# Performance work log

Hardware: AMD Instinct MI355X
Metric: run time of the kernel (lower is better)

Reference implementation:

```python
import jax, jax.numpy as jnp
import numpy as np

D = 2048
N_HID = 512
ATT = 512
BATCH = 256
L = 196


def setup_inputs() -> dict:
    key = jax.random.key(0)
    ks = jax.random.split(key, 8)
    s = 0.02
    return {
        "feature": jax.random.normal(ks[0], (BATCH, L, D), dtype=jnp.float32),
        "prev_h": jax.random.normal(ks[1], (BATCH, N_HID), dtype=jnp.float32),
        "W_enc": jax.random.normal(ks[2], (D, ATT), dtype=jnp.float32) * s,
        "b_enc": jnp.zeros((ATT,), dtype=jnp.float32),
        "W_dec": jax.random.normal(ks[3], (N_HID, ATT), dtype=jnp.float32) * s,
        "b_dec": jnp.zeros((ATT,), dtype=jnp.float32),
        "W_tot": jax.random.normal(ks[4], (ATT, 1), dtype=jnp.float32) * s,
        "b_tot": jnp.zeros((1,), dtype=jnp.float32),
    }


def reference(feature, prev_h, W_enc, b_enc, W_dec, b_dec, W_tot, b_tot):
    # att1: (N, L, A); att2: (N, A)
    att1 = jnp.einsum("nld,da->nla", feature, W_enc) + b_enc
    att2 = prev_h @ W_dec + b_dec
    att = jax.nn.relu(att1 + att2[:, None, :])          # (N, L, A)
    scores = (att @ W_tot)[..., 0] + b_tot[0]           # (N, L)
    alpha = jax.nn.softmax(scores, axis=1)              # (N, L)
    weighted_feature = jnp.einsum("nld,nl->nd", feature, alpha)  # (N, D)
    return weighted_feature, alpha
```

## Files before the change

### kernel.cpp

```cpp
#include <hip/hip_runtime.h>
#include <hip/hip_bf16.h>


typedef unsigned short u16;
typedef __attribute__((ext_vector_type(8))) short short8;
typedef __attribute__((ext_vector_type(4))) float f32x4;

#define BATCH 256
#define LQ    196
#define DDIM  2048
#define ADIM  512
#define MTOT  (BATCH * LQ)
#define WF_N  (BATCH * DDIM)
#define KQP   1032

__device__ __forceinline__ ushort4 cvt4(float4 f) {
  ushort4 r;
  r.x = __builtin_bit_cast(u16, (__bf16)f.x);
  r.y = __builtin_bit_cast(u16, (__bf16)f.y);
  r.z = __builtin_bit_cast(u16, (__bf16)f.z);
  r.w = __builtin_bit_cast(u16, (__bf16)f.w);
  return r;
}

__device__ __forceinline__ void glds16(const u16* g, u16* l) {
  __builtin_amdgcn_global_load_lds(
      (const __attribute__((address_space(1))) unsigned int*)g,
      (__attribute__((address_space(3))) unsigned int*)l, 16, 0, 0);
}

__global__ void prep_k(const float* __restrict__ W_enc, u16* __restrict__ Bst,
                       const float* __restrict__ prev_h,
                       const float* __restrict__ W_dec,
                       const float* __restrict__ b_dec,
                       const float* __restrict__ b_enc,
                       float* __restrict__ att2,
                       float* __restrict__ scores) {
  const int b = blockIdx.x, tid = threadIdx.x;
  __shared__ u16 smem[32 * 520];
  if (b < 64) {
    const int ks = b;
    for (int i4 = tid; i4 < 4096; i4 += 256) {
      int dl = i4 >> 7;
      int nn = (i4 & 127) << 2;
      float4 f = *(const float4*)(W_enc + (size_t)(ks * 32 + dl) * 512 + nn);
      *(ushort4*)(&smem[dl * 520 + nn]) = cvt4(f);
    }
    __syncthreads();
    for (int idx = tid; idx < 16384; idx += 256) {
      int kq = idx >> 12;
      int n  = (idx >> 3) & 511;
      int e  = idx & 7;
      Bst[(size_t)ks * 16384 + idx] = smem[(kq * 8 + e) * 520 + n];
    }
  } else if (b < 576) {
    const int n  = (b - 64) >> 1;
    const int c0 = ((b - 64) & 1) << 8;
    float* ph = (float*)smem;
    ph[tid]       = prev_h[n * 512 + tid];
    ph[tid + 256] = prev_h[n * 512 + tid + 256];
    __syncthreads();
    float a0 = b_dec[c0 + tid] + b_enc[c0 + tid];
    #pragma unroll 8
    for (int h = 0; h < 512; h++)
      a0 = fmaf(ph[h], W_dec[h * 512 + c0 + tid], a0);
    att2[n * 512 + c0 + tid] = a0;
  } else {
    scores[(b - 576) * 256 + tid] = 0.f;
  }
}

__global__ __launch_bounds__(256, 4) void score_gemm_k(
    const float* __restrict__ feature, const u16* __restrict__ Bst,
    const float* __restrict__ att2, const float* __restrict__ W_tot,
    float* __restrict__ scores) {
  __shared__ __align__(16) u16 sA[2][4 * KQP];
  __shared__ __align__(16) u16 sB[2][4 * KQP];
  __shared__ float sRed[2][128];

  const int tid = threadIdx.x;
  const int b = blockIdx.x;
  const int mt = (b >> 5) * 8 + (b & 7);
  const int nt = (b >> 3) & 3;
  const int r0 = mt << 7, n0 = nt << 7;
  const int wid = tid >> 6, lane = tid & 63;
  const int wgm = wid >> 1, wgn = wid & 1;
  const int quad = lane >> 4, cid = lane & 15;

  const int arow = tid >> 3, akk4 = tid & 7;
  const float* gA = feature + (size_t)(r0 + arow) * 2048 + akk4 * 4;
  const int wAoff = (akk4 >> 1) * KQP + (arow << 3) + ((akk4 & 1) << 2);

  const u16* gBlane = Bst + (size_t)wid * 4096 + ((size_t)n0 << 3) + lane * 8;

  const int abase = quad * KQP + (((wgm << 6) + cid) << 3);
  const int bbase = quad * KQP + (((wgn << 6) + cid) << 3);

  f32x4 zero = {0.f, 0.f, 0.f, 0.f};
  f32x4 acc[4][4];
  #pragma unroll
  for (int i = 0; i < 4; i++)
    #pragma unroll
    for (int j = 0; j < 4; j++) acc[i][j] = zero;

  float4 a0, a1, a2, a3;
  {
    const float* p = gA;
    a0 = *(const float4*)(p);
    a1 = *(const float4*)(p + 32 * 2048);
    a2 = *(const float4*)(p + 64 * 2048);
    a3 = *(const float4*)(p + 96 * 2048);
    u16* dst = &sB[0][wid * KQP];
    glds16(gBlane, dst);
    glds16(gBlane + 512, dst + 512);
  }

  for (int ks = 0; ks < 64; ks++) {
    const int buf = ks & 1;
    u16* wa = &sA[buf][wAoff];
    *(ushort4*)(wa)       = cvt4(a0);
    *(ushort4*)(wa + 256) = cvt4(a1);
    *(ushort4*)(wa + 512) = cvt4(a2);
    *(ushort4*)(wa + 768) = cvt4(a3);
    __syncthreads();

    if (ks < 63) {
      const float* p = gA + (ks + 1) * 32;
      a0 = *(const float4*)(p);
      a1 = *(const float4*)(p + 32 * 2048);
      a2 = *(const float4*)(p + 64 * 2048);
      a3 = *(const float4*)(p + 96 * 2048);
      const u16* src = gBlane + (size_t)(ks + 1) * 16384;
      u16* dst = &sB[buf ^ 1][wid * KQP];
      glds16(src, dst);
      glds16(src + 512, dst + 512);
    }

    const u16* sa = &sA[buf][abase];
    const u16* sb = &sB[buf][bbase];
    short8 af[4], bfr[4];
    #pragma unroll
    for (int mi = 0; mi < 4; mi++)
      af[mi] = *(const short8*)(sa + (mi << 7));
    #pragma unroll
    for (int ni = 0; ni < 4; ni++)
      bfr[ni] = *(const short8*)(sb + (ni << 7));
    #pragma unroll
    for (int mi = 0; mi < 4; mi++)
      #pragma unroll
      for (int ni = 0; ni < 4; ni++)
        acc[mi][ni] = __builtin_amdgcn_mfma_f32_16x16x32_bf16(
            af[mi], bfr[ni], acc[mi][ni], 0, 0, 0);
  }

  float wt[4];
  #pragma unroll
  for (int ni = 0; ni < 4; ni++)
    wt[ni] = W_tot[n0 + (wgn << 6) + ni * 16 + cid];

  #pragma unroll
  for (int mi = 0; mi < 4; mi++) {
    #pragma unroll
    for (int reg = 0; reg < 4; reg++) {
      int row_local = (wgm << 6) + mi * 16 + quad * 4 + reg;
      int row_flat = r0 + row_local;
      int nb = row_flat / 196;
      const float* a2r = att2 + nb * 512 + n0 + (wgn << 6);
      float s = 0.f;
      #pragma unroll
      for (int ni = 0; ni < 4; ni++) {
        float v = acc[mi][ni][reg] + a2r[ni * 16 + cid];
        s += fmaxf(v, 0.f) * wt[ni];
      }
      s += __shfl_xor(s, 1); s += __shfl_xor(s, 2);
      s += __shfl_xor(s, 4); s += __shfl_xor(s, 8);
      if (cid == 0) sRed[wgn][row_local] = s;
    }
  }
  __syncthreads();
  if (tid < 128) atomicAdd(&scores[r0 + tid], sRed[0][tid] + sRed[1][tid]);
}

__global__ void softmax_k(const float* __restrict__ scores,
                          float* __restrict__ alpha) {
  const int n = blockIdx.x, tid = threadIdx.x;
  __shared__ float red[8];
  float s = (tid < LQ) ? scores[n * LQ + tid] : -1e30f;
  float m = s;
  for (int o = 32; o; o >>= 1) m = fmaxf(m, __shfl_xor(m, o));
  if ((tid & 63) == 0) red[tid >> 6] = m;
  __syncthreads();
  m = fmaxf(fmaxf(red[0], red[1]), fmaxf(red[2], red[3]));
  float e = (tid < LQ) ? __expf(s - m) : 0.f;
  float t = e;
  for (int o = 32; o; o >>= 1) t += __shfl_xor(t, o);
  if ((tid & 63) == 0) red[4 + (tid >> 6)] = t;
  __syncthreads();
  t = red[4] + red[5] + red[6] + red[7];
  if (tid < LQ) alpha[n * LQ + tid] = e / t;
}

__global__ void wsum_k(const float* __restrict__ feature,
                       const float* __restrict__ alpha,
                       float* __restrict__ out) {
  const int n = blockIdx.x >> 1, half = blockIdx.x & 1;
  const int tid = threadIdx.x;
  __shared__ float al[LQ];
  if (tid < LQ) al[tid] = alpha[n * LQ + tid];
  __syncthreads();
  const float* fp = feature + (size_t)n * LQ * DDIM + half * 1024 + tid * 4;
  float4 acc = {0.f, 0.f, 0.f, 0.f};
  #pragma unroll 8
  for (int l = 0; l < LQ; l++) {
    float a = al[l];
    float4 f = *(const float4*)(fp + (size_t)l * DDIM);
    acc.x = fmaf(a, f.x, acc.x); acc.y = fmaf(a, f.y, acc.y);
    acc.z = fmaf(a, f.z, acc.z); acc.w = fmaf(a, f.w, acc.w);
  }
  *(float4*)(out + n * DDIM + half * 1024 + tid * 4) = acc;
}

extern "C" void kernel_launch(void* const* d_in, const int* in_sizes, int n_in,
                              void* d_out, int out_size, void* d_ws, size_t ws_size,
                              hipStream_t stream) {
  const float* feature = (const float*)d_in[0];
  const float* prev_h  = (const float*)d_in[1];
  const float* W_enc   = (const float*)d_in[2];
  const float* b_enc   = (const float*)d_in[3];
  const float* W_dec   = (const float*)d_in[4];
  const float* b_dec   = (const float*)d_in[5];
  const float* W_tot   = (const float*)d_in[6];

  float* out   = (float*)d_out;
  float* wf    = out;
  float* alpha = out + WF_N;

  char* ws = (char*)d_ws;
  u16*   Bst    = (u16*)ws;
  float* att2   = (float*)(ws + (2u << 20));
  float* scores = (float*)(ws + (2u << 20) + (512u << 10));

  prep_k<<<772, 256, 0, stream>>>(W_enc, Bst, prev_h, W_dec, b_dec, b_enc,
                                  att2, scores);
  score_gemm_k<<<1568, 256, 0, stream>>>(feature, Bst, att2, W_tot, scores);
  softmax_k<<<256, 256, 0, stream>>>(scores, alpha);
  wsum_k<<<512, 256, 0, stream>>>(feature, alpha, wf);
}
```

Baseline: 751.5 us.

## Load A operand directly into MFMA registers, bypassing shared memory staging

The feature (A) tile no longer goes through LDS. Each lane now loads its own MFMA fragment rows straight from global memory into registers and converts them to bf16 in place, which removes the LDS writes and reads for A. The cost is duplicated global reads: each feature row is fetched by both wgn warps, so L2/global traffic for A doubles. Register pressure also rises, which is why launch bounds drop occupancy from 4 to 3 blocks per SM.

Result: slower. 1.142 ms (+52.0%).

```diff
diff --git a/kernel.cpp b/kernel.cpp
--- a/kernel.cpp
+++ b/kernel.cpp
@@ -20,6 +20,19 @@
   r.y = __builtin_bit_cast(u16, (__bf16)f.y);
   r.z = __builtin_bit_cast(u16, (__bf16)f.z);
   r.w = __builtin_bit_cast(u16, (__bf16)f.w);
+  return r;
+}
+
+__device__ __forceinline__ short8 cvt8(float4 a, float4 b) {
+  short8 r;
+  r[0] = (short)__builtin_bit_cast(u16, (__bf16)a.x);
+  r[1] = (short)__builtin_bit_cast(u16, (__bf16)a.y);
+  r[2] = (short)__builtin_bit_cast(u16, (__bf16)a.z);
+  r[3] = (short)__builtin_bit_cast(u16, (__bf16)a.w);
+  r[4] = (short)__builtin_bit_cast(u16, (__bf16)b.x);
+  r[5] = (short)__builtin_bit_cast(u16, (__bf16)b.y);
+  r[6] = (short)__builtin_bit_cast(u16, (__bf16)b.z);
+  r[7] = (short)__builtin_bit_cast(u16, (__bf16)b.w);
   return r;
 }
 
@@ -70,11 +83,10 @@
   }
 }
 
-__global__ __launch_bounds__(256, 4) void score_gemm_k(
+__global__ __launch_bounds__(256, 3) void score_gemm_k(
     const float* __restrict__ feature, const u16* __restrict__ Bst,
     const float* __restrict__ att2, const float* __restrict__ W_tot,
     float* __restrict__ scores) {
-  __shared__ __align__(16) u16 sA[2][4 * KQP];
   __shared__ __align__(16) u16 sB[2][4 * KQP];
   __shared__ float sRed[2][128];
 
@@ -87,13 +99,11 @@
   const int wgm = wid >> 1, wgn = wid & 1;
   const int quad = lane >> 4, cid = lane & 15;
 
-  const int arow = tid >> 3, akk4 = tid & 7;
-  const float* gA = feature + (size_t)(r0 + arow) * 2048 + akk4 * 4;
-  const int wAoff = (akk4 >> 1) * KQP + (arow << 3) + ((akk4 & 1) << 2);
+  const float* gAf =
+      feature + (size_t)(r0 + (wgm << 6) + cid) * 2048 + (quad << 3);
 
   const u16* gBlane = Bst + (size_t)wid * 4096 + ((size_t)n0 << 3) + lane * 8;
 
-  const int abase = quad * KQP + (((wgm << 6) + cid) << 3);
   const int bbase = quad * KQP + (((wgn << 6) + cid) << 3);
 
   f32x4 zero = {0.f, 0.f, 0.f, 0.f};
@@ -103,13 +113,16 @@
     #pragma unroll
     for (int j = 0; j < 4; j++) acc[i][j] = zero;
 
-  float4 a0, a1, a2, a3;
+  float4 aF0, aF1, aF2, aF3, aF4, aF5, aF6, aF7;
   {
-    const float* p = gA;
-    a0 = *(const float4*)(p);
-    a1 = *(const float4*)(p + 32 * 2048);
-    a2 = *(const float4*)(p + 64 * 2048);
-    a3 = *(const float4*)(p + 96 * 2048);
+    aF0 = *(const float4*)(gAf);
+    aF1 = *(const float4*)(gAf + 4);
+    aF2 = *(const float4*)(gAf + 16 * 2048);
+    aF3 = *(const float4*)(gAf + 16 * 2048 + 4);
+    aF4 = *(const float4*)(gAf + 32 * 2048);
+    aF5 = *(const float4*)(gAf + 32 * 2048 + 4);
+    aF6 = *(const float4*)(gAf + 48 * 2048);
+    aF7 = *(const float4*)(gAf + 48 * 2048 + 4);
     u16* dst = &sB[0][wid * KQP];
     glds16(gBlane, dst);
     glds16(gBlane + 512, dst + 512);
@@ -117,31 +130,32 @@
 
   for (int ks = 0; ks < 64; ks++) {
     const int buf = ks & 1;
-    u16* wa = &sA[buf][wAoff];
-    *(ushort4*)(wa)       = cvt4(a0);
-    *(ushort4*)(wa + 256) = cvt4(a1);
-    *(ushort4*)(wa + 512) = cvt4(a2);
-    *(ushort4*)(wa + 768) = cvt4(a3);
     __syncthreads();
 
+    short8 af[4];
+    af[0] = cvt8(aF0, aF1);
+    af[1] = cvt8(aF2, aF3);
+    af[2] = cvt8(aF4, aF5);
+    af[3] = cvt8(aF6, aF7);
+
     if (ks < 63) {
-      const float* p = gA + (ks + 1) * 32;
-      a0 = *(const float4*)(p);
-      a1 = *(const float4*)(p + 32 * 2048);
-      a2 = *(const float4*)(p + 64 * 2048);
-      a3 = *(const float4*)(p + 96 * 2048);
+      const float* p = gAf + (ks + 1) * 32;
+      aF0 = *(const float4*)(p);
+      aF1 = *(const float4*)(p + 4);
+      aF2 = *(const float4*)(p + 16 * 2048);
+      aF3 = *(const float4*)(p + 16 * 2048 + 4);
+      aF4 = *(const float4*)(p + 32 * 2048);
+      aF5 = *(const float4*)(p + 32 * 2048 + 4);
+      aF6 = *(const float4*)(p + 48 * 2048);
+      aF7 = *(const float4*)(p + 48 * 2048 + 4);
       const u16* src = gBlane + (size_t)(ks + 1) * 16384;
       u16* dst = &sB[buf ^ 1][wid * KQP];
       glds16(src, dst);
       glds16(src + 512, dst + 512);
     }
 
-    const u16* sa = &sA[buf][abase];
     const u16* sb = &sB[buf][bbase];
-    short8 af[4], bfr[4];
-    #pragma unroll
-    for (int mi = 0; mi < 4; mi++)
-      af[mi] = *(const short8*)(sa + (mi << 7));
+    short8 bfr[4];
     #pragma unroll
     for (int ni = 0; ni < 4; ni++)
       bfr[ni] = *(const short8*)(sb + (ni << 7));
```

## Deepen score GEMM pipeline with triple A register prefetch and quad B buffers

Applied to the files above, without the earlier changes.

Restructures the score GEMM main loop so each K-step's fp32 A tile is loaded three steps ahead into rotating register sets. B tiles are copied into LDS two steps ahead using four LDS buffers. Each step uses one barrier with a hand-written partial vmcnt wait instead of waiting for all loads, and the loop is unrolled by 12 with a peeled tail. This is meant to hide global-memory latency behind the MFMA work. In exchange it uses more registers and LDS, so launch bounds drop from 4 to 3 blocks per CU, and the manual waitcnt count is fragile.

Result: slower. 935.0 us (+24.4%).

```diff
diff --git a/kernel.cpp b/kernel.cpp
--- a/kernel.cpp
+++ b/kernel.cpp
@@ -14,12 +14,13 @@
 #define WF_N  (BATCH * DDIM)
 #define KQP   1032
 
+__device__ __forceinline__ u16 bfc(float f) {
+  return __builtin_bit_cast(u16, (__bf16)f);
+}
+
 __device__ __forceinline__ ushort4 cvt4(float4 f) {
   ushort4 r;
-  r.x = __builtin_bit_cast(u16, (__bf16)f.x);
-  r.y = __builtin_bit_cast(u16, (__bf16)f.y);
-  r.z = __builtin_bit_cast(u16, (__bf16)f.z);
-  r.w = __builtin_bit_cast(u16, (__bf16)f.w);
+  r.x = bfc(f.x); r.y = bfc(f.y); r.z = bfc(f.z); r.w = bfc(f.w);
   return r;
 }
 
@@ -70,12 +71,12 @@
   }
 }
 
-__global__ __launch_bounds__(256, 4) void score_gemm_k(
+__global__ __launch_bounds__(256, 3) void score_gemm_k(
     const float* __restrict__ feature, const u16* __restrict__ Bst,
     const float* __restrict__ att2, const float* __restrict__ W_tot,
     float* __restrict__ scores) {
   __shared__ __align__(16) u16 sA[2][4 * KQP];
-  __shared__ __align__(16) u16 sB[2][4 * KQP];
+  __shared__ __align__(16) u16 sB[4][4 * KQP];
   __shared__ float sRed[2][128];
 
   const int tid = threadIdx.x;
@@ -103,55 +104,92 @@
     #pragma unroll
     for (int j = 0; j < 4; j++) acc[i][j] = zero;
 
-  float4 a0, a1, a2, a3;
-  {
-    const float* p = gA;
-    a0 = *(const float4*)(p);
-    a1 = *(const float4*)(p + 32 * 2048);
-    a2 = *(const float4*)(p + 64 * 2048);
-    a3 = *(const float4*)(p + 96 * 2048);
-    u16* dst = &sB[0][wid * KQP];
-    glds16(gBlane, dst);
-    glds16(gBlane + 512, dst + 512);
-  }
-
-  for (int ks = 0; ks < 64; ks++) {
-    const int buf = ks & 1;
-    u16* wa = &sA[buf][wAoff];
-    *(ushort4*)(wa)       = cvt4(a0);
-    *(ushort4*)(wa + 256) = cvt4(a1);
-    *(ushort4*)(wa + 512) = cvt4(a2);
-    *(ushort4*)(wa + 768) = cvt4(a3);
-    __syncthreads();
-
-    if (ks < 63) {
-      const float* p = gA + (ks + 1) * 32;
-      a0 = *(const float4*)(p);
-      a1 = *(const float4*)(p + 32 * 2048);
-      a2 = *(const float4*)(p + 64 * 2048);
-      a3 = *(const float4*)(p + 96 * 2048);
-      const u16* src = gBlane + (size_t)(ks + 1) * 16384;
-      u16* dst = &sB[buf ^ 1][wid * KQP];
-      glds16(src, dst);
-      glds16(src + 512, dst + 512);
-    }
-
-    const u16* sa = &sA[buf][abase];
-    const u16* sb = &sB[buf][bbase];
-    short8 af[4], bfr[4];
-    #pragma unroll
-    for (int mi = 0; mi < 4; mi++)
-      af[mi] = *(const short8*)(sa + (mi << 7));
-    #pragma unroll
-    for (int ni = 0; ni < 4; ni++)
-      bfr[ni] = *(const short8*)(sb + (ni << 7));
-    #pragma unroll
-    for (int mi = 0; mi < 4; mi++)
-      #pragma unroll
-      for (int ni = 0; ni < 4; ni++)
-        acc[mi][ni] = __builtin_amdgcn_mfma_f32_16x16x32_bf16(
-            af[mi], bfr[ni], acc[mi][ni], 0, 0, 0);
-  }
+  float4 aS0_0, aS0_1, aS0_2, aS0_3;
+  float4 aS1_0, aS1_1, aS1_2, aS1_3;
+  float4 aS2_0, aS2_1, aS2_2, aS2_3;
+
+#define LOAD_A(SET, KS) do {                                              \
+    const float* p_ = gA + (size_t)(KS) * 32;                             \
+    aS##SET##_0 = *(const float4*)(p_);                                   \
+    aS##SET##_1 = *(const float4*)(p_ + 32 * 2048);                       \
+    aS##SET##_2 = *(const float4*)(p_ + 64 * 2048);                       \
+    aS##SET##_3 = *(const float4*)(p_ + 96 * 2048);                       \
+  } while (0)
+
+#define STAGE_A(SET, ABUF) do {                                           \
+    u16* wa_ = &sA[ABUF][wAoff];                                          \
+    *(ushort4*)(wa_)       = cvt4(aS##SET##_0);                           \
+    *(ushort4*)(wa_ + 256) = cvt4(aS##SET##_1);                           \
+    *(ushort4*)(wa_ + 512) = cvt4(aS##SET##_2);                           \
+    *(ushort4*)(wa_ + 768) = cvt4(aS##SET##_3);                           \
+  } while (0)
+
+#define GLDS_B2(KS, BUFI) do {                                            \
+    const u16* src_ = gBlane + (size_t)(KS) * 16384;                      \
+    u16* dst_ = &sB[BUFI][wid * KQP];                                     \
+    glds16(src_, dst_);                                                   \
+    glds16(src_ + 512, dst_ + 512);                                       \
+  } while (0)
+
+#define COMPUTE(ABUF, BBUF) do {                                          \
+    const u16* sa_ = &sA[ABUF][abase];                                    \
+    const u16* sb_ = &sB[BBUF][bbase];                                    \
+    short8 af_[4], bf_[4];                                                \
+    _Pragma("unroll")                                                     \
+    for (int mi = 0; mi < 4; mi++)                                        \
+      af_[mi] = *(const short8*)(sa_ + (mi << 7));                        \
+    _Pragma("unroll")                                                     \
+    for (int ni = 0; ni < 4; ni++)                                        \
+      bf_[ni] = *(const short8*)(sb_ + (ni << 7));                        \
+    _Pragma("unroll")                                                     \
+    for (int mi = 0; mi < 4; mi++)                                        \
+      _Pragma("unroll")                                                   \
+      for (int ni = 0; ni < 4; ni++)                                      \
+        acc[mi][ni] = __builtin_amdgcn_mfma_f32_16x16x32_bf16(            \
+            af_[mi], bf_[ni], acc[mi][ni], 0, 0, 0);                      \
+  } while (0)
+
+#define ITER_BODY(KS, SET, ABUF, BRD, BWR) do {                           \
+    STAGE_A(SET, ABUF);                                                   \
+    GLDS_B2((KS) + 2, BWR);                                               \
+    LOAD_A(SET, (KS) + 3);                                                \
+    asm volatile("s_waitcnt vmcnt(16) lgkmcnt(0)" ::: "memory");          \
+    __builtin_amdgcn_s_barrier();                                         \
+    COMPUTE(ABUF, BRD);                                                   \
+  } while (0)
+
+  GLDS_B2(0, 0);
+  GLDS_B2(1, 1);
+  LOAD_A(0, 0);
+  LOAD_A(1, 1);
+  LOAD_A(2, 2);
+
+  #pragma unroll 1
+  for (int kb = 0; kb < 60; kb += 12) {
+    ITER_BODY(kb + 0,  0, 0, 0, 2);
+    ITER_BODY(kb + 1,  1, 1, 1, 3);
+    ITER_BODY(kb + 2,  2, 0, 2, 0);
+    ITER_BODY(kb + 3,  0, 1, 3, 1);
+    ITER_BODY(kb + 4,  1, 0, 0, 2);
+    ITER_BODY(kb + 5,  2, 1, 1, 3);
+    ITER_BODY(kb + 6,  0, 0, 2, 0);
+    ITER_BODY(kb + 7,  1, 1, 3, 1);
+    ITER_BODY(kb + 8,  2, 0, 0, 2);
+    ITER_BODY(kb + 9,  0, 1, 1, 3);
+    ITER_BODY(kb + 10, 1, 0, 2, 0);
+    ITER_BODY(kb + 11, 2, 1, 3, 1);
+  }
+  ITER_BODY(60, 0, 0, 0, 2);
+
+  STAGE_A(1, 1); GLDS_B2(63, 3); __syncthreads(); COMPUTE(1, 1);
+  STAGE_A(2, 0);                 __syncthreads(); COMPUTE(0, 2);
+  STAGE_A(0, 1);                 __syncthreads(); COMPUTE(1, 3);
+
+#undef ITER_BODY
+#undef COMPUTE
+#undef GLDS_B2
+#undef STAGE_A
+#undef LOAD_A
 
   float wt[4];
   #pragma unroll
```
